# Performance work log

Measured on AMD Instinct MI355X. Metric: run time of the kernel, lower is better.

## Reference

```python
import jax, jax.numpy as jnp
import numpy as np

K = 3  # number of nearest neighbors for interpolation
BIG = 1e10  # masks out cross-batch pairs in the distance matrix


def setup_inputs() -> dict:
    key = jax.random.key(0)
    ks = jax.random.split(key, 8)
    N, Ns, C, Cs, B = 4096, 16384, 256, 128, 4
    Din, H = C + Cs, 256
    return {
        "x": jax.random.normal(ks[0], (N, C), dtype=jnp.float32),
        "pos": jax.random.normal(ks[1], (N, 3), dtype=jnp.float32),
        "batch": jnp.sort(jax.random.randint(ks[2], (N,), 0, B)),
        "x_skip": jax.random.normal(ks[3], (Ns, Cs), dtype=jnp.float32),
        "pos_skip": jax.random.normal(ks[4], (Ns, 3), dtype=jnp.float32),
        "batch_skip": jnp.sort(jax.random.randint(ks[5], (Ns,), 0, B)),
        "W1": jax.random.normal(ks[6], (Din, H), dtype=jnp.float32) * (1.0 / np.sqrt(Din)),
        "b1": jnp.zeros((H,), dtype=jnp.float32),
        "W2": jax.random.normal(ks[7], (H, H), dtype=jnp.float32) * (1.0 / np.sqrt(H)),
        "b2": jnp.zeros((H,), dtype=jnp.float32),
    }


def reference(x, pos, batch, x_skip, pos_skip, batch_skip, W1, b1, W2, b2):
    # knn_interpolate: squared distances from each fine point to all coarse points,
    # masked so neighbors only come from the same batch element.
    d2 = jnp.sum((pos_skip[:, None, :] - pos[None, :, :]) ** 2, axis=-1)  # [Ns, N]
    d2 = jnp.where(batch_skip[:, None] != batch[None, :], BIG, d2)
    neg_d2, idx = jax.lax.top_k(-d2, K)          # k smallest distances, [Ns, K]
    w = 1.0 / jnp.clip(-neg_d2, 1e-16)           # inverse-squared-distance weights
    num = jnp.sum(x[idx] * w[..., None], axis=1)  # [Ns, C] weighted gather-reduce
    y = num / jnp.sum(w, axis=1, keepdims=True)
    # concat skip features, then MLP (Linear-ReLU-Linear-ReLU)
    y = jnp.concatenate([y, x_skip], axis=1)      # [Ns, C + Cs]
    h = jax.nn.relu(y @ W1 + b1)
    out = jax.nn.relu(h @ W2 + b2)
    return (out, pos_skip, batch_skip)
```

## Files before the change

### kernel.cpp

```cpp
#include <hip/hip_runtime.h>
#include <stdint.h>

#define NPTS   4096
#define NSKIP  16384
#define CCH    256
#define CSK    128
#define DIN    384
#define HDIM   256
#define BIGF   1e10f

typedef unsigned short u16;
typedef __attribute__((ext_vector_type(8))) short short8;
typedef __attribute__((ext_vector_type(4))) float floatx4;

__device__ __forceinline__ u16 f2bf(float f) {
    union { float f; uint32_t u; } c; c.f = f;
    uint32_t u = c.u;
    return (u16)((u + 0x7FFFu + ((u >> 16) & 1u)) >> 16);
}

__device__ __forceinline__ double pkkey(float d, int j) {
    return __hiloint2double(__float_as_int(d), j);
}

__global__ __launch_bounds__(256) void prep_knn_kernel(
    const float* __restrict__ W1, const float* __restrict__ W2,
    u16* __restrict__ W1p, u16* __restrict__ W2p,
    const float* __restrict__ pos, const int* __restrict__ batch,
    const float* __restrict__ pos_skip, const int* __restrict__ batch_skip,
    int* __restrict__ idx3, float* __restrict__ w3)
{
    const int bid = blockIdx.x;
    const int t = threadIdx.x;

    if (bid < 80) {
        const float* W = (bid < 48) ? W1 : W2;
        u16* Wp       = (bid < 48) ? W1p : W2p;
        const int KT  = (bid < 48) ? 12 : 8;
        const int g   = ((bid < 48) ? bid : (bid - 48)) * 256 + t;

        const int lane = g & 63;
        const int kt = (g >> 6) % KT;
        const int nt = (g >> 6) / KT;
        const int kbase = kt * 32 + (lane >> 4) * 8;
        const int n = nt * 16 + (lane & 15);
        u16 v[8];
#pragma unroll
        for (int j = 0; j < 8; ++j) v[j] = f2bf(W[(size_t)(kbase + j) * HDIM + n]);
#pragma unroll
        for (int j = 0; j < 8; ++j) Wp[(size_t)g * 8 + j] = v[j];
        return;
    }

    __shared__ int sRange[5];
    if (t < 5) {
        int lo = 0, hi = NPTS;
        while (lo < hi) {
            const int m = (lo + hi) >> 1;
            if (batch[m] < t) lo = m + 1; else hi = m;
        }
        sRange[t] = lo;
    }
    __syncthreads();

    const int i = (bid - 80) * 8 + (t >> 5);
    const int sub = t & 31;
    const int b = batch_skip[i];
    const int start = sRange[b], end = sRange[b + 1];

    const float px = pos_skip[i * 3 + 0];
    const float py = pos_skip[i * 3 + 1];
    const float pz = pos_skip[i * 3 + 2];

    const double BIGKEY = pkkey(BIGF, 0x7FFFFFFF);
    double k0 = BIGKEY, k1 = BIGKEY, k2 = BIGKEY;

    for (int j = start + sub; j < end; j += 32) {
        const float qx = pos[j * 3 + 0];
        const float qy = pos[j * 3 + 1];
        const float qz = pos[j * 3 + 2];
        const float dx = __fsub_rn(px, qx);
        const float dy = __fsub_rn(py, qy);
        const float dz = __fsub_rn(pz, qz);
        const float dd = __fadd_rn(__fadd_rn(__fmul_rn(dx, dx), __fmul_rn(dy, dy)),
                                   __fmul_rn(dz, dz));
        const double kk = pkkey(dd, j);
        const double u0 = fmax(k0, kk); k0 = fmin(k0, kk);
        const double u1 = fmax(k1, u0); k1 = fmin(k1, u0);
        k2 = fmin(k2, u1);
    }

#pragma unroll
    for (int m = 1; m < 32; m <<= 1) {
        const double o0 = __shfl_xor(k0, m);
        const double o1 = __shfl_xor(k1, m);
        const double o2 = __shfl_xor(k2, m);
        double u0 = fmax(k0, o0); k0 = fmin(k0, o0);
        double u1 = fmax(k1, u0); k1 = fmin(k1, u0);
        k2 = fmin(k2, u1);
        u1 = fmax(k1, o1); k1 = fmin(k1, o1);
        k2 = fmin(k2, u1);
        k2 = fmin(k2, o2);
    }

    if (sub == 0) {
        const float d0 = __int_as_float(__double2hiint(k0));
        const float d1 = __int_as_float(__double2hiint(k1));
        const float d2 = __int_as_float(__double2hiint(k2));
        const float w0 = 1.0f / fmaxf(d0, 1e-16f);
        const float w1 = 1.0f / fmaxf(d1, 1e-16f);
        const float w2 = 1.0f / fmaxf(d2, 1e-16f);
        const float inv = 1.0f / (w0 + w1 + w2);
        idx3[i * 3 + 0] = __double2loint(k0);
        idx3[i * 3 + 1] = __double2loint(k1);
        idx3[i * 3 + 2] = __double2loint(k2);
        w3[i * 3 + 0] = w0 * inv; w3[i * 3 + 1] = w1 * inv; w3[i * 3 + 2] = w2 * inv;
    }
}

__global__ __launch_bounds__(256) void fused_mlp_kernel(
    const float* __restrict__ x, const float* __restrict__ x_skip,
    const int* __restrict__ idx3, const float* __restrict__ w3,
    const u16* __restrict__ W1p, const float* __restrict__ b1,
    const u16* __restrict__ W2p, const float* __restrict__ b2,
    const float* __restrict__ pos_skip, const int* __restrict__ batch_skip,
    float* __restrict__ out)
{
    __shared__ u16 sA[32 * 392];
    __shared__ float sOut[32 * 256];
    const int t = threadIdx.x;
    const int row0 = blockIdx.x * 32;
    const int wave = t >> 6, lane = t & 63;
    const int quad = lane >> 4, ml = lane & 15;

#pragma unroll
    for (int half = 0; half < 2; ++half) {
        int i0a[4], i1a[4], i2a[4];
        float wa[4], wb[4], wc[4];
#pragma unroll
        for (int k = 0; k < 4; ++k) {
            const int g = t + 256 * (half * 4 + k);
            const int R = row0 + (g >> 6);
            i0a[k] = idx3[R * 3 + 0]; i1a[k] = idx3[R * 3 + 1]; i2a[k] = idx3[R * 3 + 2];
            wa[k] = w3[R * 3 + 0]; wb[k] = w3[R * 3 + 1]; wc[k] = w3[R * 3 + 2];
        }
        float4 v0[4], v1[4], v2[4];
#pragma unroll
        for (int k = 0; k < 4; ++k) {
            const int g = t + 256 * (half * 4 + k);
            const int c4 = g & 63;
            v0[k] = *(const float4*)(x + (size_t)i0a[k] * CCH + c4 * 4);
            v1[k] = *(const float4*)(x + (size_t)i1a[k] * CCH + c4 * 4);
            v2[k] = *(const float4*)(x + (size_t)i2a[k] * CCH + c4 * 4);
        }
#pragma unroll
        for (int k = 0; k < 4; ++k) {
            const int g = t + 256 * (half * 4 + k);
            const int row = g >> 6, c4 = g & 63;
            const float a  = wa[k] * v0[k].x + wb[k] * v1[k].x + wc[k] * v2[k].x;
            const float bq = wa[k] * v0[k].y + wb[k] * v1[k].y + wc[k] * v2[k].y;
            const float cq = wa[k] * v0[k].z + wb[k] * v1[k].z + wc[k] * v2[k].z;
            const float dq = wa[k] * v0[k].w + wb[k] * v1[k].w + wc[k] * v2[k].w;
            uint2 pk;
            pk.x = (uint32_t)f2bf(a)  | ((uint32_t)f2bf(bq) << 16);
            pk.y = (uint32_t)f2bf(cq) | ((uint32_t)f2bf(dq) << 16);
            *(uint2*)(sA + row * 392 + c4 * 4) = pk;
        }
    }
    {
        float4 vs[4];
#pragma unroll
        for (int k = 0; k < 4; ++k) {
            const int g = t + 256 * k;
            const int row = g >> 5, c4 = g & 31;
            vs[k] = *(const float4*)(x_skip + (size_t)(row0 + row) * CSK + c4 * 4);
        }
#pragma unroll
        for (int k = 0; k < 4; ++k) {
            const int g = t + 256 * k;
            const int row = g >> 5, c4 = g & 31;
            uint2 pk;
            pk.x = (uint32_t)f2bf(vs[k].x) | ((uint32_t)f2bf(vs[k].y) << 16);
            pk.y = (uint32_t)f2bf(vs[k].z) | ((uint32_t)f2bf(vs[k].w) << 16);
            *(uint2*)(sA + row * 392 + CCH + c4 * 4) = pk;
        }
    }
    __syncthreads();

    floatx4 acc[2][4] = {};
    {
        const u16* aA = sA + ml * 392 + quad * 8;
        short8 bbuf[2][4];
#pragma unroll
        for (int nt = 0; nt < 4; ++nt) {
            bbuf[0][nt] = *(const short8*)(W1p + (size_t)(((wave * 4 + nt) * 12 + 0) * 64 + lane) * 8);
            bbuf[1][nt] = *(const short8*)(W1p + (size_t)(((wave * 4 + nt) * 12 + 1) * 64 + lane) * 8);
        }
#pragma unroll
        for (int kt = 0; kt < 12; ++kt) {
            short8 use[4];
#pragma unroll
            for (int nt = 0; nt < 4; ++nt) use[nt] = bbuf[kt & 1][nt];
            if (kt + 2 < 12) {
#pragma unroll
                for (int nt = 0; nt < 4; ++nt)
                    bbuf[kt & 1][nt] = *(const short8*)(W1p + (size_t)(((wave * 4 + nt) * 12 + kt + 2) * 64 + lane) * 8);
            }
            short8 a0 = *(const short8*)(aA + kt * 32);
            short8 a1 = *(const short8*)(aA + 16 * 392 + kt * 32);
#pragma unroll
            for (int nt = 0; nt < 4; ++nt) {
                acc[0][nt] = __builtin_amdgcn_mfma_f32_16x16x32_bf16(a0, use[nt], acc[0][nt], 0, 0, 0);
                acc[1][nt] = __builtin_amdgcn_mfma_f32_16x16x32_bf16(a1, use[nt], acc[1][nt], 0, 0, 0);
            }
        }
    }
    __syncthreads();

    short8 b2buf[2][4];
#pragma unroll
    for (int nt = 0; nt < 4; ++nt) {
        b2buf[0][nt] = *(const short8*)(W2p + (size_t)(((wave * 4 + nt) * 8 + 0) * 64 + lane) * 8);
        b2buf[1][nt] = *(const short8*)(W2p + (size_t)(((wave * 4 + nt) * 8 + 1) * 64 + lane) * 8);
    }

#pragma unroll
    for (int mt = 0; mt < 2; ++mt) {
#pragma unroll
        for (int nt = 0; nt < 4; ++nt) {
            const int n = (wave * 4 + nt) * 16 + ml;
            const float bv = b1[n];
#pragma unroll
            for (int r = 0; r < 4; ++r) {
                const int m = mt * 16 + quad * 4 + r;
                sA[m * 264 + n] = f2bf(fmaxf(acc[mt][nt][r] + bv, 0.0f));
            }
        }
    }
    __syncthreads();

    floatx4 acc2[2][4] = {};
    {
        const u16* aH = sA + ml * 264 + quad * 8;
#pragma unroll
        for (int kt = 0; kt < 8; ++kt) {
            short8 use[4];
#pragma unroll
            for (int nt = 0; nt < 4; ++nt) use[nt] = b2buf[kt & 1][nt];
            if (kt + 2 < 8) {
#pragma unroll
                for (int nt = 0; nt < 4; ++nt)
                    b2buf[kt & 1][nt] = *(const short8*)(W2p + (size_t)(((wave * 4 + nt) * 8 + kt + 2) * 64 + lane) * 8);
            }
            short8 a0 = *(const short8*)(aH + kt * 32);
            short8 a1 = *(const short8*)(aH + 16 * 264 + kt * 32);
#pragma unroll
            for (int nt = 0; nt < 4; ++nt) {
                acc2[0][nt] = __builtin_amdgcn_mfma_f32_16x16x32_bf16(a0, use[nt], acc2[0][nt], 0, 0, 0);
                acc2[1][nt] = __builtin_amdgcn_mfma_f32_16x16x32_bf16(a1, use[nt], acc2[1][nt], 0, 0, 0);
            }
        }
    }

#pragma unroll
    for (int mt = 0; mt < 2; ++mt) {
#pragma unroll
        for (int nt = 0; nt < 4; ++nt) {
            const int n = (wave * 4 + nt) * 16 + ml;
            const float bv = b2[n];
#pragma unroll
            for (int r = 0; r < 4; ++r) {
                const int m = mt * 16 + quad * 4 + r;
                sOut[m * 256 + n] = fmaxf(acc2[mt][nt][r] + bv, 0.0f);
            }
        }
    }
    __syncthreads();
    {
        float* dst = out + (size_t)row0 * HDIM;
#pragma unroll
        for (int k = 0; k < 8; ++k) {
            const int e = t + 256 * k;
            *(float4*)(dst + e * 4) = *(const float4*)(sOut + e * 4);
        }
    }

    if (t < 128) {
        const int e = blockIdx.x * 128 + t;
        const size_t base = (size_t)NSKIP * HDIM;
        if (e < NSKIP * 3) out[base + e] = pos_skip[e];
        else               out[base + e] = (float)batch_skip[e - NSKIP * 3];
    }
}

extern "C" void kernel_launch(void* const* d_in, const int* in_sizes, int n_in,
                              void* d_out, int out_size, void* d_ws, size_t ws_size,
                              hipStream_t stream) {
    const float* x         = (const float*)d_in[0];
    const float* pos       = (const float*)d_in[1];
    const int*   batch     = (const int*)d_in[2];
    const float* x_skip    = (const float*)d_in[3];
    const float* pos_skip  = (const float*)d_in[4];
    const int*   batch_skip= (const int*)d_in[5];
    const float* W1        = (const float*)d_in[6];
    const float* b1        = (const float*)d_in[7];
    const float* W2        = (const float*)d_in[8];
    const float* b2        = (const float*)d_in[9];
    float* out = (float*)d_out;

    char* ws = (char*)d_ws;
    u16*    W1p   = (u16*)ws;
    u16*    W2p   = (u16*)(ws + 196608);
    int*    idx3  = (int*)(ws + 327680);
    float*  w3    = (float*)(ws + 524288);

    prep_knn_kernel<<<80 + NSKIP / 8, 256, 0, stream>>>(W1, W2, W1p, W2p,
                                                        pos, batch,
                                                        pos_skip, batch_skip,
                                                        idx3, w3);
    fused_mlp_kernel<<<NSKIP / 32, 256, 0, stream>>>(x, x_skip, idx3, w3,
                                                     W1p, b1, W2p, b2,
                                                     pos_skip, batch_skip, out);
}
```

Baseline: 118.5 us.

## Use 8 waves per block in fused MLP and drop weight prefetch buffers

The fused MLP kernel launches 512 threads instead of 256, so each wave computes two 16-column N tiles instead of four. The gather and skip-load loops are re-indexed to spread over twice as many threads. The register double-buffered prefetch of W1/W2 fragments is removed in favor of loading each fragment directly before its MFMA. The intent is more waves in flight and fewer registers per thread to hide gather and weight-load latency, at the cost of losing explicit software prefetch and keeping the k-loop rolled.

```diff
diff --git a/kernel.cpp b/kernel.cpp
--- a/kernel.cpp
+++ b/kernel.cpp
@@ -118,7 +118,7 @@
     }
 }
 
-__global__ __launch_bounds__(256) void fused_mlp_kernel(
+__global__ __launch_bounds__(512) void fused_mlp_kernel(
     const float* __restrict__ x, const float* __restrict__ x_skip,
     const int* __restrict__ idx3, const float* __restrict__ w3,
     const u16* __restrict__ W1p, const float* __restrict__ b1,
@@ -133,13 +133,12 @@
     const int wave = t >> 6, lane = t & 63;
     const int quad = lane >> 4, ml = lane & 15;
 
-#pragma unroll
-    for (int half = 0; half < 2; ++half) {
+    {
         int i0a[4], i1a[4], i2a[4];
         float wa[4], wb[4], wc[4];
 #pragma unroll
         for (int k = 0; k < 4; ++k) {
-            const int g = t + 256 * (half * 4 + k);
+            const int g = t + 512 * k;
             const int R = row0 + (g >> 6);
             i0a[k] = idx3[R * 3 + 0]; i1a[k] = idx3[R * 3 + 1]; i2a[k] = idx3[R * 3 + 2];
             wa[k] = w3[R * 3 + 0]; wb[k] = w3[R * 3 + 1]; wc[k] = w3[R * 3 + 2];
@@ -147,7 +146,7 @@
         float4 v0[4], v1[4], v2[4];
 #pragma unroll
         for (int k = 0; k < 4; ++k) {
-            const int g = t + 256 * (half * 4 + k);
+            const int g = t + 512 * k;
             const int c4 = g & 63;
             v0[k] = *(const float4*)(x + (size_t)i0a[k] * CCH + c4 * 4);
             v1[k] = *(const float4*)(x + (size_t)i1a[k] * CCH + c4 * 4);
@@ -155,7 +154,7 @@
         }
 #pragma unroll
         for (int k = 0; k < 4; ++k) {
-            const int g = t + 256 * (half * 4 + k);
+            const int g = t + 512 * k;
             const int row = g >> 6, c4 = g & 63;
             const float a  = wa[k] * v0[k].x + wb[k] * v1[k].x + wc[k] * v2[k].x;
             const float bq = wa[k] * v0[k].y + wb[k] * v1[k].y + wc[k] * v2[k].y;
@@ -168,16 +167,16 @@
         }
     }
     {
-        float4 vs[4];
-#pragma unroll
-        for (int k = 0; k < 4; ++k) {
-            const int g = t + 256 * k;
+        float4 vs[2];
+#pragma unroll
+        for (int k = 0; k < 2; ++k) {
+            const int g = t + 512 * k;
             const int row = g >> 5, c4 = g & 31;
             vs[k] = *(const float4*)(x_skip + (size_t)(row0 + row) * CSK + c4 * 4);
         }
 #pragma unroll
-        for (int k = 0; k < 4; ++k) {
-            const int g = t + 256 * k;
+        for (int k = 0; k < 2; ++k) {
+            const int g = t + 512 * k;
             const int row = g >> 5, c4 = g & 31;
             uint2 pk;
             pk.x = (uint32_t)f2bf(vs[k].x) | ((uint32_t)f2bf(vs[k].y) << 16);
@@ -187,48 +186,28 @@
     }
     __syncthreads();
 
-    floatx4 acc[2][4] = {};
+    floatx4 acc[2][2] = {};
     {
         const u16* aA = sA + ml * 392 + quad * 8;
-        short8 bbuf[2][4];
-#pragma unroll
-        for (int nt = 0; nt < 4; ++nt) {
-            bbuf[0][nt] = *(const short8*)(W1p + (size_t)(((wave * 4 + nt) * 12 + 0) * 64 + lane) * 8);
-            bbuf[1][nt] = *(const short8*)(W1p + (size_t)(((wave * 4 + nt) * 12 + 1) * 64 + lane) * 8);
-        }
-#pragma unroll
         for (int kt = 0; kt < 12; ++kt) {
-            short8 use[4];
-#pragma unroll
-            for (int nt = 0; nt < 4; ++nt) use[nt] = bbuf[kt & 1][nt];
-            if (kt + 2 < 12) {
-#pragma unroll
-                for (int nt = 0; nt < 4; ++nt)
-                    bbuf[kt & 1][nt] = *(const short8*)(W1p + (size_t)(((wave * 4 + nt) * 12 + kt + 2) * 64 + lane) * 8);
-            }
             short8 a0 = *(const short8*)(aA + kt * 32);
             short8 a1 = *(const short8*)(aA + 16 * 392 + kt * 32);
 #pragma unroll
-            for (int nt = 0; nt < 4; ++nt) {
-                acc[0][nt] = __builtin_amdgcn_mfma_f32_16x16x32_bf16(a0, use[nt], acc[0][nt], 0, 0, 0);
-                acc[1][nt] = __builtin_amdgcn_mfma_f32_16x16x32_bf16(a1, use[nt], acc[1][nt], 0, 0, 0);
-            }
-        }
-    }
-    __syncthreads();
-
-    short8 b2buf[2][4];
-#pragma unroll
-    for (int nt = 0; nt < 4; ++nt) {
-        b2buf[0][nt] = *(const short8*)(W2p + (size_t)(((wave * 4 + nt) * 8 + 0) * 64 + lane) * 8);
-        b2buf[1][nt] = *(const short8*)(W2p + (size_t)(((wave * 4 + nt) * 8 + 1) * 64 + lane) * 8);
-    }
+            for (int nt = 0; nt < 2; ++nt) {
+                const int ntile = wave * 2 + nt;
+                short8 bfr = *(const short8*)(W1p + (size_t)((ntile * 12 + kt) * 64 + lane) * 8);
+                acc[0][nt] = __builtin_amdgcn_mfma_f32_16x16x32_bf16(a0, bfr, acc[0][nt], 0, 0, 0);
+                acc[1][nt] = __builtin_amdgcn_mfma_f32_16x16x32_bf16(a1, bfr, acc[1][nt], 0, 0, 0);
+            }
+        }
+    }
+    __syncthreads();
 
 #pragma unroll
     for (int mt = 0; mt < 2; ++mt) {
 #pragma unroll
-        for (int nt = 0; nt < 4; ++nt) {
-            const int n = (wave * 4 + nt) * 16 + ml;
+        for (int nt = 0; nt < 2; ++nt) {
+            const int n = (wave * 2 + nt) * 16 + ml;
             const float bv = b1[n];
 #pragma unroll
             for (int r = 0; r < 4; ++r) {
@@ -239,25 +218,18 @@
     }
     __syncthreads();
 
-    floatx4 acc2[2][4] = {};
+    floatx4 acc2[2][2] = {};
     {
         const u16* aH = sA + ml * 264 + quad * 8;
-#pragma unroll
         for (int kt = 0; kt < 8; ++kt) {
-            short8 use[4];
-#pragma unroll
-            for (int nt = 0; nt < 4; ++nt) use[nt] = b2buf[kt & 1][nt];
-            if (kt + 2 < 8) {
-#pragma unroll
-                for (int nt = 0; nt < 4; ++nt)
-                    b2buf[kt & 1][nt] = *(const short8*)(W2p + (size_t)(((wave * 4 + nt) * 8 + kt + 2) * 64 + lane) * 8);
-            }
             short8 a0 = *(const short8*)(aH + kt * 32);
             short8 a1 = *(const short8*)(aH + 16 * 264 + kt * 32);
 #pragma unroll
-            for (int nt = 0; nt < 4; ++nt) {
-                acc2[0][nt] = __builtin_amdgcn_mfma_f32_16x16x32_bf16(a0, use[nt], acc2[0][nt], 0, 0, 0);
-                acc2[1][nt] = __builtin_amdgcn_mfma_f32_16x16x32_bf16(a1, use[nt], acc2[1][nt], 0, 0, 0);
+            for (int nt = 0; nt < 2; ++nt) {
+                const int ntile = wave * 2 + nt;
+                short8 bfr = *(const short8*)(W2p + (size_t)((ntile * 8 + kt) * 64 + lane) * 8);
+                acc2[0][nt] = __builtin_amdgcn_mfma_f32_16x16x32_bf16(a0, bfr, acc2[0][nt], 0, 0, 0);
+                acc2[1][nt] = __builtin_amdgcn_mfma_f32_16x16x32_bf16(a1, bfr, acc2[1][nt], 0, 0, 0);
             }
         }
     }
@@ -265,8 +237,8 @@
 #pragma unroll
     for (int mt = 0; mt < 2; ++mt) {
 #pragma unroll
-        for (int nt = 0; nt < 4; ++nt) {
-            const int n = (wave * 4 + nt) * 16 + ml;
+        for (int nt = 0; nt < 2; ++nt) {
+            const int n = (wave * 2 + nt) * 16 + ml;
             const float bv = b2[n];
 #pragma unroll
             for (int r = 0; r < 4; ++r) {
@@ -279,8 +251,8 @@
     {
         float* dst = out + (size_t)row0 * HDIM;
 #pragma unroll
-        for (int k = 0; k < 8; ++k) {
-            const int e = t + 256 * k;
+        for (int k = 0; k < 4; ++k) {
+            const int e = t + 512 * k;
             *(float4*)(dst + e * 4) = *(const float4*)(sOut + e * 4);
         }
     }
@@ -318,7 +290,7 @@
                                                         pos, batch,
                                                         pos_skip, batch_skip,
                                                         idx3, w3);
-    fused_mlp_kernel<<<NSKIP / 32, 256, 0, stream>>>(x, x_skip, idx3, w3,
+    fused_mlp_kernel<<<NSKIP / 32, 512, 0, stream>>>(x, x_skip, idx3, w3,
                                                      W1p, b1, W2p, b2,
                                                      pos_skip, batch_skip, out);
 }
```

Result: faster. 114.4 us (-3.5%).
